# Kernel tuning notes

Hardware: AMD Instinct MI355X
Metric: run time of the kernel (lower is better)

Reference implementation:

```python
import jax, jax.numpy as jnp
import numpy as np

NF4_LUT = jnp.array([-1.0, -0.6961928009986877, -0.5250730514526367, -0.39491719007492065,
                     -0.28444138169288635, -0.18477343022823334, -0.08820830285549164, 0.0,
                     0.07107656449079514, 0.14263366162776947, 0.22430233657360077,
                     0.3203405737876892, 0.4407068192958832, 0.5905631184577942,
                     0.796090841293335, 1.0], dtype=jnp.float32)

BLOCK_SIZE = 64
OUT_FEATURES = 11008
IN_FEATURES = 4096


def dequantize_nf4(packed, absmax, out_shape):
    # packed: (O, I//2) int codes 0..255; absmax: (O, num_blocks)
    higher = packed // 16
    lower = packed % 16
    unpacked = jnp.stack([lower, higher], axis=-1).reshape(out_shape)  # (O, I)
    dequant = NF4_LUT[unpacked]  # LUT gather -> fp32 (O, I)
    O, I = out_shape
    # block-wise absmax scale
    dequant = (dequant.reshape(O, I // BLOCK_SIZE, BLOCK_SIZE) * absmax[:, :, None]).reshape(O, I)
    return dequant


def setup_inputs() -> dict:
    key = jax.random.key(0)
    k1, k2, k3, k4 = jax.random.split(key, 4)
    x = jax.random.normal(k1, (4, 2048, IN_FEATURES), dtype=jnp.float32)
    weight = jax.random.randint(k2, (OUT_FEATURES, IN_FEATURES // 2), 0, 256, dtype=jnp.int32)
    absmax = jax.random.uniform(k3, (OUT_FEATURES, IN_FEATURES // BLOCK_SIZE), dtype=jnp.float32)
    bias = jax.random.normal(k4, (OUT_FEATURES,), dtype=jnp.float32)
    return {"x": x, "weight": weight, "absmax": absmax, "bias": bias}


def reference(x, weight, absmax, bias):
    w = dequantize_nf4(weight, absmax, (OUT_FEATURES, IN_FEATURES))  # (O, I)
    # F.linear: y = x @ w.T + bias
    return jnp.einsum('bsi,oi->bso', x, w) + bias
```

## Files before the change

kernel.cpp:

```cpp
#include <hip/hip_runtime.h>

#define IN_F 4096
#define OUT_F 11008

typedef __attribute__((ext_vector_type(8))) short bf16x8;
typedef __attribute__((ext_vector_type(4))) float f32x4;
typedef __attribute__((ext_vector_type(4))) unsigned short us4;
typedef __attribute__((ext_vector_type(8))) unsigned short us8;

__device__ __forceinline__ unsigned short f2bf(float f) {
  unsigned int u = __float_as_uint(f);
  u += 0x7FFFu + ((u >> 16) & 1u);
  return (unsigned short)(u >> 16);
}

__global__ __launch_bounds__(256) void cvt_x(const float* __restrict__ X,
                                             unsigned short* __restrict__ Xb, int n8) {
  for (int i = blockIdx.x * blockDim.x + threadIdx.x; i < n8;
       i += gridDim.x * blockDim.x) {
    const float4 a = reinterpret_cast<const float4*>(X)[2 * i];
    const float4 b = reinterpret_cast<const float4*>(X)[2 * i + 1];
    us8 h;
    h[0] = f2bf(a.x); h[1] = f2bf(a.y); h[2] = f2bf(a.z); h[3] = f2bf(a.w);
    h[4] = f2bf(b.x); h[5] = f2bf(b.y); h[6] = f2bf(b.z); h[7] = f2bf(b.w);
    reinterpret_cast<us8*>(Xb)[i] = h;
  }
}

__global__ __launch_bounds__(256) void dequant_w(const int* __restrict__ Wp,
                                                 const float* __restrict__ Amax,
                                                 unsigned short* __restrict__ Wb, int n4) {
  __shared__ float lutS[16];
  if (threadIdx.x < 16) {
    const float lut[16] = {-1.0f, -0.6961928009986877f, -0.5250730514526367f,
        -0.39491719007492065f, -0.28444138169288635f, -0.18477343022823334f,
        -0.08820830285549164f, 0.0f, 0.07107656449079514f, 0.14263366162776947f,
        0.22430233657360077f, 0.3203405737876892f, 0.4407068192958832f,
        0.5905631184577942f, 0.796090841293335f, 1.0f};
    lutS[threadIdx.x] = lut[threadIdx.x];
  }
  __syncthreads();
  for (int i = blockIdx.x * blockDim.x + threadIdx.x; i < n4;
       i += gridDim.x * blockDim.x) {
    const int j = i * 4;
    const int row = j >> 11;
    const int coli = j & 2047;
    const float am = Amax[row * (IN_F / 64) + (coli >> 5)];
    const int4 pk = reinterpret_cast<const int4*>(Wp)[i];
    us8 h; int c;
    c = pk.x & 255; h[0] = f2bf(lutS[c & 15] * am); h[1] = f2bf(lutS[c >> 4] * am);
    c = pk.y & 255; h[2] = f2bf(lutS[c & 15] * am); h[3] = f2bf(lutS[c >> 4] * am);
    c = pk.z & 255; h[4] = f2bf(lutS[c & 15] * am); h[5] = f2bf(lutS[c >> 4] * am);
    c = pk.w & 255; h[6] = f2bf(lutS[c & 15] * am); h[7] = f2bf(lutS[c >> 4] * am);
    reinterpret_cast<us8*>(Wb)[i] = h;
  }
}

#define MF(a, b, c) __builtin_amdgcn_mfma_f32_16x16x32_bf16(a, b, c, 0, 0, 0)
#define GLDS(src, dst) __builtin_amdgcn_global_load_lds( \
    (const __attribute__((address_space(1))) void*)(src), \
    (__attribute__((address_space(3))) void*)(dst), 16, 0, 0)
#define FENCE asm volatile("" ::: "memory")
#define BAR do { FENCE; __builtin_amdgcn_s_barrier(); FENCE; } while (0)
#define VM8 asm volatile("s_waitcnt vmcnt(8)" ::: "memory")
#define VM4 asm volatile("s_waitcnt vmcnt(4)" ::: "memory")
#define VM0 asm volatile("s_waitcnt vmcnt(0)" ::: "memory")

__global__ __launch_bounds__(512, 2) void gemm256(
    const unsigned short* __restrict__ A,
    const unsigned short* __restrict__ B,
    const float* __restrict__ Bias, float* __restrict__ Out, int M) {
  extern __shared__ unsigned short sm[];
  unsigned short* LA = sm;
  unsigned short* LB = sm + 32768;

  const int tid = threadIdx.x;
  const int l = tid & 63;
  const int wid = tid >> 6;

  const int Mb = M / 256;
  const int Nb = OUT_F / 256;
  const int cpx = (Mb * Nb) >> 3;
  const int bid = (blockIdx.x & 7) * cpx + (blockIdx.x >> 3);
  const int m0 = (bid % Mb) * 256;
  const int n0 = (bid / Mb) * 256;

  const int rh = (l & 15) >> 1;
  const int cph = (((l & 1) << 2) + (l >> 4)) ^ rh;
  const int aoff = (((wid >> 2) * 64) + rh) * 64 + cph * 8;
  const int boff = (((wid & 3) * 32) + rh) * 64 + cph * 8;

  const int cc = (l & 7) ^ (l >> 3);
  const int R0 = 2 * (wid * 16 + (l >> 3)) + (cc >> 2);
  const long chb = (long)(cc & 3) * 16;
  const char* pA0 = (const char*)A + ((size_t)(m0 + R0) * IN_F) * 2 + chb;
  const char* pA1 = (const char*)A + ((size_t)(m0 + R0 + 16) * IN_F) * 2 + chb;
  const char* pB0 = (const char*)B + ((size_t)(n0 + R0) * IN_F) * 2 + chb;
  const char* pB1 = (const char*)B + ((size_t)(n0 + R0 + 16) * IN_F) * 2 + chb;
  const int dq0 = wid * 1024;
  const int dq1 = wid * 1024 + 512;

#define STAGE_A(tt) do { const int s_ = ((tt) & 3) * 8192; const size_t ko_ = (size_t)(tt) * 64; \
    GLDS(pA0 + ko_, LA + s_ + dq0); GLDS(pA1 + ko_, LA + s_ + dq1); } while (0)
#define STAGE_B(tt) do { const int s_ = ((tt) & 3) * 8192; const size_t ko_ = (size_t)(tt) * 64; \
    GLDS(pB0 + ko_, LB + s_ + dq0); GLDS(pB1 + ko_, LB + s_ + dq1); } while (0)

  f32x4 acc[8][4];
#pragma unroll
  for (int i = 0; i < 8; ++i)
#pragma unroll
    for (int j = 0; j < 4; ++j) acc[i][j] = {0.f, 0.f, 0.f, 0.f};

  STAGE_A(0); STAGE_B(0); STAGE_A(1); STAGE_B(1); STAGE_A(2); STAGE_B(2);

#define TILE(t, STG, VMW) do { \
  VMW; \
  BAR; \
  const int sb = ((t) & 3) * 8192; \
  bf16x8 a0, a1, a2, a3, a4, a5, a6, a7, b0, b1, b2, b3; \
  a0 = *(const bf16x8*)(LA + sb + aoff); \
  a1 = *(const bf16x8*)(LA + sb + aoff + 512); \
  a2 = *(const bf16x8*)(LA + sb + aoff + 1024); \
  a3 = *(const bf16x8*)(LA + sb + aoff + 1536); \
  b0 = *(const bf16x8*)(LB + sb + boff); \
  b1 = *(const bf16x8*)(LB + sb + boff + 512); \
  b2 = *(const bf16x8*)(LB + sb + boff + 1024); \
  b3 = *(const bf16x8*)(LB + sb + boff + 1536); \
  a4 = *(const bf16x8*)(LA + sb + aoff + 2048); \
  a5 = *(const bf16x8*)(LA + sb + aoff + 2560); \
  a6 = *(const bf16x8*)(LA + sb + aoff + 3072); \
  a7 = *(const bf16x8*)(LA + sb + aoff + 3584); \
  __builtin_amdgcn_s_setprio(1); \
  acc[0][0] = MF(a0, b0, acc[0][0]); acc[0][1] = MF(a0, b1, acc[0][1]); \
  acc[0][2] = MF(a0, b2, acc[0][2]); acc[0][3] = MF(a0, b3, acc[0][3]); \
  acc[1][0] = MF(a1, b0, acc[1][0]); acc[1][1] = MF(a1, b1, acc[1][1]); \
  acc[1][2] = MF(a1, b2, acc[1][2]); acc[1][3] = MF(a1, b3, acc[1][3]); \
  acc[2][0] = MF(a2, b0, acc[2][0]); acc[2][1] = MF(a2, b1, acc[2][1]); \
  acc[2][2] = MF(a2, b2, acc[2][2]); acc[2][3] = MF(a2, b3, acc[2][3]); \
  acc[3][0] = MF(a3, b0, acc[3][0]); acc[3][1] = MF(a3, b1, acc[3][1]); \
  acc[3][2] = MF(a3, b2, acc[3][2]); acc[3][3] = MF(a3, b3, acc[3][3]); \
  __builtin_amdgcn_s_setprio(0); \
  if (STG) { STAGE_A((t) + 3); STAGE_B((t) + 3); } \
  __builtin_amdgcn_s_setprio(1); \
  acc[4][0] = MF(a4, b0, acc[4][0]); acc[4][1] = MF(a4, b1, acc[4][1]); \
  acc[4][2] = MF(a4, b2, acc[4][2]); acc[4][3] = MF(a4, b3, acc[4][3]); \
  acc[5][0] = MF(a5, b0, acc[5][0]); acc[5][1] = MF(a5, b1, acc[5][1]); \
  acc[5][2] = MF(a5, b2, acc[5][2]); acc[5][3] = MF(a5, b3, acc[5][3]); \
  acc[6][0] = MF(a6, b0, acc[6][0]); acc[6][1] = MF(a6, b1, acc[6][1]); \
  acc[6][2] = MF(a6, b2, acc[6][2]); acc[6][3] = MF(a6, b3, acc[6][3]); \
  acc[7][0] = MF(a7, b0, acc[7][0]); acc[7][1] = MF(a7, b1, acc[7][1]); \
  acc[7][2] = MF(a7, b2, acc[7][2]); acc[7][3] = MF(a7, b3, acc[7][3]); \
  __builtin_amdgcn_s_setprio(0); \
} while (0)

  for (int t = 0; t < 125; ++t) { TILE(t, 1, VM8); }
  TILE(125, 0, VM8);
  TILE(126, 0, VM4);
  TILE(127, 0, VM0);

  const int crow = m0 + (wid >> 2) * 128 + ((l >> 4) << 2);
  const int ccol = n0 + (wid & 3) * 64 + (l & 15);
#pragma unroll
  for (int nf = 0; nf < 4; ++nf) {
    const float bv = Bias[ccol + nf * 16];
#pragma unroll
    for (int f = 0; f < 8; ++f)
#pragma unroll
      for (int rg = 0; rg < 4; ++rg)
        Out[(size_t)(crow + f * 16 + rg) * OUT_F + ccol + nf * 16] = acc[f][nf][rg] + bv;
  }
}

__global__ __launch_bounds__(256, 2) void nf4_gemm_fused(
    const float* __restrict__ X, const int* __restrict__ Wp,
    const float* __restrict__ Amax, const float* __restrict__ Bias,
    float* __restrict__ Out, int M) {
  __shared__ unsigned short As[128 * 64];
  __shared__ unsigned short Bs[128 * 64];
  __shared__ float lutS[16];

  const int t = threadIdx.x;
  const int l = t & 63;
  const int wid = t >> 6;

  if (t < 16) {
    const float lut[16] = {-1.0f, -0.6961928009986877f, -0.5250730514526367f,
        -0.39491719007492065f, -0.28444138169288635f, -0.18477343022823334f,
        -0.08820830285549164f, 0.0f, 0.07107656449079514f, 0.14263366162776947f,
        0.22430233657360077f, 0.3203405737876892f, 0.4407068192958832f,
        0.5905631184577942f, 0.796090841293335f, 1.0f};
    lutS[t] = lut[t];
  }

  const int ntile = OUT_F / 128;
  const int m0 = (blockIdx.x / ntile) * 128;
  const int n0 = (blockIdx.x % ntile) * 128;

  const int ar = t >> 4;
  const int ac4 = t & 15;
  const int br = t >> 3;
  const int bg = t & 7;
  const int wm = (wid >> 1) * 64;
  const int wn = (wid & 1) * 64;

  f32x4 acc[4][4];
#pragma unroll
  for (int i = 0; i < 4; ++i)
#pragma unroll
    for (int j = 0; j < 4; ++j) acc[i][j] = {0.f, 0.f, 0.f, 0.f};

  __syncthreads();

  for (int k0 = 0; k0 < IN_F; k0 += 64) {
#pragma unroll
    for (int p = 0; p < 8; ++p) {
      const int r = p * 16 + ar;
      const float4 v = *reinterpret_cast<const float4*>(
          X + (size_t)(m0 + r) * IN_F + k0 + ac4 * 4);
      us4 h;
      h[0] = f2bf(v.x); h[1] = f2bf(v.y); h[2] = f2bf(v.z); h[3] = f2bf(v.w);
      const int byte = r * 128 + ((ac4 * 8) ^ ((r & 7) << 4));
      *reinterpret_cast<us4*>(reinterpret_cast<char*>(As) + byte) = h;
    }
#pragma unroll
    for (int p = 0; p < 4; ++p) {
      const int r = p * 32 + br;
      const float amv = Amax[(size_t)(n0 + r) * (IN_F / 64) + (k0 >> 6)];
      const int4 pk = *reinterpret_cast<const int4*>(
          Wp + (size_t)(n0 + r) * (IN_F / 2) + (k0 >> 1) + bg * 4);
      us8 h;
      {
        int c;
        c = pk.x & 255; h[0] = f2bf(lutS[c & 15] * amv); h[1] = f2bf(lutS[c >> 4] * amv);
        c = pk.y & 255; h[2] = f2bf(lutS[c & 15] * amv); h[3] = f2bf(lutS[c >> 4] * amv);
        c = pk.z & 255; h[4] = f2bf(lutS[c & 15] * amv); h[5] = f2bf(lutS[c >> 4] * amv);
        c = pk.w & 255; h[6] = f2bf(lutS[c & 15] * amv); h[7] = f2bf(lutS[c >> 4] * amv);
      }
      const int byte = r * 128 + ((bg * 16) ^ ((r & 7) << 4));
      *reinterpret_cast<us8*>(reinterpret_cast<char*>(Bs) + byte) = h;
    }
    __syncthreads();

#pragma unroll
    for (int kk = 0; kk < 64; kk += 32) {
      bf16x8 af[4], bfv[4];
      const int kb = (kk + ((l >> 4) << 3)) * 2;
#pragma unroll
      for (int i = 0; i < 4; ++i) {
        const int row = wm + i * 16 + (l & 15);
        af[i] = *reinterpret_cast<const bf16x8*>(
            reinterpret_cast<const char*>(As) + row * 128 + (kb ^ ((row & 7) << 4)));
      }
#pragma unroll
      for (int j = 0; j < 4; ++j) {
        const int row = wn + j * 16 + (l & 15);
        bfv[j] = *reinterpret_cast<const bf16x8*>(
            reinterpret_cast<const char*>(Bs) + row * 128 + (kb ^ ((row & 7) << 4)));
      }
#pragma unroll
      for (int i = 0; i < 4; ++i)
#pragma unroll
        for (int j = 0; j < 4; ++j)
          acc[i][j] = __builtin_amdgcn_mfma_f32_16x16x32_bf16(af[i], bfv[j], acc[i][j], 0, 0, 0);
    }
    __syncthreads();
  }

  const int crow0 = m0 + wm + ((l >> 4) << 2);
  const int ccol0 = n0 + wn + (l & 15);
#pragma unroll
  for (int j = 0; j < 4; ++j) {
    const float bv = Bias[ccol0 + j * 16];
#pragma unroll
    for (int i = 0; i < 4; ++i)
#pragma unroll
      for (int rg = 0; rg < 4; ++rg)
        Out[(size_t)(crow0 + i * 16 + rg) * OUT_F + ccol0 + j * 16] = acc[i][j][rg] + bv;
  }
}

extern "C" void kernel_launch(void* const* d_in, const int* in_sizes, int n_in,
                              void* d_out, int out_size, void* d_ws, size_t ws_size,
                              hipStream_t stream) {
  const float* X = (const float*)d_in[0];
  const int* Wp = (const int*)d_in[1];
  const float* Amax = (const float*)d_in[2];
  const float* Bias = (const float*)d_in[3];
  float* Out = (float*)d_out;

  const int M = in_sizes[0] / IN_F;
  const size_t needX = (size_t)M * IN_F * 2;
  const size_t needW = (size_t)OUT_F * IN_F * 2;
  const int grid256 = (M / 256) * (OUT_F / 256);

  if (ws_size >= needX + needW && (M % 256) == 0 && (grid256 & 7) == 0) {
    unsigned short* Xb = (unsigned short*)d_ws;
    unsigned short* Wb = Xb + (size_t)M * IN_F;
    (void)hipFuncSetAttribute(reinterpret_cast<const void*>(gemm256),
                              hipFuncAttributeMaxDynamicSharedMemorySize, 131072);
    cvt_x<<<2048, 256, 0, stream>>>(X, Xb, M * (IN_F / 8));
    dequant_w<<<2048, 256, 0, stream>>>(Wp, Amax, Wb, OUT_F * (IN_F / 8));
    gemm256<<<grid256, 512, 131072, stream>>>(Xb, Wb, Bias, Out, M);
  } else {
    const int grid = (M / 128) * (OUT_F / 128);
    nf4_gemm_fused<<<grid, 256, 0, stream>>>(X, Wp, Amax, Bias, Out, M);
  }
}
```

Measured before the change: 850.4 us.

## Restructure bf16 GEMM main loop into 128-wide K tiles with interleaved staging

```diff
diff --git a/kernel.cpp b/kernel.cpp
--- a/kernel.cpp
+++ b/kernel.cpp
@@ -62,17 +62,18 @@
     (__attribute__((address_space(3))) void*)(dst), 16, 0, 0)
 #define FENCE asm volatile("" ::: "memory")
 #define BAR do { FENCE; __builtin_amdgcn_s_barrier(); FENCE; } while (0)
-#define VM8 asm volatile("s_waitcnt vmcnt(8)" ::: "memory")
-#define VM4 asm volatile("s_waitcnt vmcnt(4)" ::: "memory")
+#define VM6 asm volatile("s_waitcnt vmcnt(6)" ::: "memory")
 #define VM0 asm volatile("s_waitcnt vmcnt(0)" ::: "memory")
+#define VMNOP do {} while (0)
+#define P1 __builtin_amdgcn_s_setprio(1)
+#define P0 __builtin_amdgcn_s_setprio(0)
 
 __global__ __launch_bounds__(512, 2) void gemm256(
     const unsigned short* __restrict__ A,
     const unsigned short* __restrict__ B,
     const float* __restrict__ Bias, float* __restrict__ Out, int M) {
   extern __shared__ unsigned short sm[];
-  unsigned short* LA = sm;
-  unsigned short* LB = sm + 32768;
+  char* const smc = (char*)sm;
 
   const int tid = threadIdx.x;
   const int l = tid & 63;
@@ -85,25 +86,71 @@
   const int m0 = (bid % Mb) * 256;
   const int n0 = (bid / Mb) * 256;
 
-  const int rh = (l & 15) >> 1;
-  const int cph = (((l & 1) << 2) + (l >> 4)) ^ rh;
-  const int aoff = (((wid >> 2) * 64) + rh) * 64 + cph * 8;
-  const int boff = (((wid & 3) * 32) + rh) * 64 + cph * 8;
-
-  const int cc = (l & 7) ^ (l >> 3);
-  const int R0 = 2 * (wid * 16 + (l >> 3)) + (cc >> 2);
-  const long chb = (long)(cc & 3) * 16;
-  const char* pA0 = (const char*)A + ((size_t)(m0 + R0) * IN_F) * 2 + chb;
-  const char* pA1 = (const char*)A + ((size_t)(m0 + R0 + 16) * IN_F) * 2 + chb;
-  const char* pB0 = (const char*)B + ((size_t)(n0 + R0) * IN_F) * 2 + chb;
-  const char* pB1 = (const char*)B + ((size_t)(n0 + R0 + 16) * IN_F) * 2 + chb;
-  const int dq0 = wid * 1024;
-  const int dq1 = wid * 1024 + 512;
-
-#define STAGE_A(tt) do { const int s_ = ((tt) & 3) * 8192; const size_t ko_ = (size_t)(tt) * 64; \
-    GLDS(pA0 + ko_, LA + s_ + dq0); GLDS(pA1 + ko_, LA + s_ + dq1); } while (0)
-#define STAGE_B(tt) do { const int s_ = ((tt) & 3) * 8192; const size_t ko_ = (size_t)(tt) * 64; \
-    GLDS(pB0 + ko_, LB + s_ + dq0); GLDS(pB1 + ko_, LB + s_ + dq1); } while (0)
+  const int lv = (l & 15) * 64 + (((l >> 4) ^ ((l >> 2) & 3)) * 16);
+  const int aLane = (wid >> 2) * 8192 + lv;
+  const int bLane = 32768 + (wid & 3) * 4096 + lv;
+
+  const int rq = tid >> 2;
+  const int cs = (tid & 3) ^ ((tid >> 4) & 3);
+  const unsigned short* gAs = A + (size_t)(m0 + rq) * IN_F + cs * 8;
+  const unsigned short* gBs = B + (size_t)(n0 + rq) * IN_F + cs * 8;
+
+#define SA(t, kh) do { \
+    unsigned short* d_ = sm + (size_t)((((t) & 1) * 4096) + (kh) * 1024 + wid * 64) * 8; \
+    const unsigned short* s_ = gAs + (size_t)(t) * 64 + (kh) * 32; \
+    GLDS(s_, d_); GLDS(s_ + 524288, d_ + 4096); } while (0)
+#define SB(t, kh) do { \
+    unsigned short* d_ = sm + (size_t)((((t) & 1) * 4096) + 2048 + (kh) * 1024 + wid * 64) * 8; \
+    const unsigned short* s_ = gBs + (size_t)(t) * 64 + (kh) * 32; \
+    GLDS(s_, d_); GLDS(s_ + 524288, d_ + 4096); } while (0)
+
+#define RD_A(kh) do { const char* p_ = LAb + (kh) * 16384; \
+    a0 = *(const bf16x8*)(p_);        a1 = *(const bf16x8*)(p_ + 1024); \
+    a2 = *(const bf16x8*)(p_ + 2048); a3 = *(const bf16x8*)(p_ + 3072); \
+    a4 = *(const bf16x8*)(p_ + 4096); a5 = *(const bf16x8*)(p_ + 5120); \
+    a6 = *(const bf16x8*)(p_ + 6144); a7 = *(const bf16x8*)(p_ + 7168); } while (0)
+#define RD_B01(kh) do { const char* p_ = LBb + (kh) * 16384; \
+    b0 = *(const bf16x8*)(p_); b1 = *(const bf16x8*)(p_ + 1024); } while (0)
+#define RD_B23(kh) do { const char* p_ = LBb + (kh) * 16384 + 2048; \
+    b2 = *(const bf16x8*)(p_); b3 = *(const bf16x8*)(p_ + 1024); } while (0)
+
+#define MM16_01(B0, B1) do { \
+    acc[0][0]=MF(a0,B0,acc[0][0]); acc[0][1]=MF(a0,B1,acc[0][1]); \
+    acc[1][0]=MF(a1,B0,acc[1][0]); acc[1][1]=MF(a1,B1,acc[1][1]); \
+    acc[2][0]=MF(a2,B0,acc[2][0]); acc[2][1]=MF(a2,B1,acc[2][1]); \
+    acc[3][0]=MF(a3,B0,acc[3][0]); acc[3][1]=MF(a3,B1,acc[3][1]); \
+    acc[4][0]=MF(a4,B0,acc[4][0]); acc[4][1]=MF(a4,B1,acc[4][1]); \
+    acc[5][0]=MF(a5,B0,acc[5][0]); acc[5][1]=MF(a5,B1,acc[5][1]); \
+    acc[6][0]=MF(a6,B0,acc[6][0]); acc[6][1]=MF(a6,B1,acc[6][1]); \
+    acc[7][0]=MF(a7,B0,acc[7][0]); acc[7][1]=MF(a7,B1,acc[7][1]); } while (0)
+#define MM16_23(B2, B3) do { \
+    acc[0][2]=MF(a0,B2,acc[0][2]); acc[0][3]=MF(a0,B3,acc[0][3]); \
+    acc[1][2]=MF(a1,B2,acc[1][2]); acc[1][3]=MF(a1,B3,acc[1][3]); \
+    acc[2][2]=MF(a2,B2,acc[2][2]); acc[2][3]=MF(a2,B3,acc[2][3]); \
+    acc[3][2]=MF(a3,B2,acc[3][2]); acc[3][3]=MF(a3,B3,acc[3][3]); \
+    acc[4][2]=MF(a4,B2,acc[4][2]); acc[4][3]=MF(a4,B3,acc[4][3]); \
+    acc[5][2]=MF(a5,B2,acc[5][2]); acc[5][3]=MF(a5,B3,acc[5][3]); \
+    acc[6][2]=MF(a6,B2,acc[6][2]); acc[6][3]=MF(a6,B3,acc[6][3]); \
+    acc[7][2]=MF(a7,B2,acc[7][2]); acc[7][3]=MF(a7,B3,acc[7][3]); } while (0)
+
+#define KTILE(T, S1, S2, VMW) do { \
+    const char* LAb = smc + (((T) & 1) << 16) + aLane; \
+    const char* LBb = smc + (((T) & 1) << 16) + bLane; \
+    bf16x8 a0, a1, a2, a3, a4, a5, a6, a7, b0, b1, b2, b3; \
+    RD_A(0); RD_B01(0); \
+    if (S1) SB((T) + 1, 1); \
+    BAR; P1; MM16_01(b0, b1); P0; BAR; \
+    RD_B23(0); \
+    if (S2) SA((T) + 2, 0); \
+    BAR; P1; MM16_23(b2, b3); P0; BAR; \
+    RD_A(1); RD_B01(1); \
+    if (S2) SB((T) + 2, 0); \
+    BAR; P1; MM16_01(b0, b1); P0; BAR; \
+    RD_B23(1); \
+    if (S2) SA((T) + 2, 1); \
+    VMW; \
+    BAR; P1; MM16_23(b2, b3); P0; BAR; \
+  } while (0)
 
   f32x4 acc[8][4];
 #pragma unroll
@@ -111,52 +158,13 @@
 #pragma unroll
     for (int j = 0; j < 4; ++j) acc[i][j] = {0.f, 0.f, 0.f, 0.f};
 
-  STAGE_A(0); STAGE_B(0); STAGE_A(1); STAGE_B(1); STAGE_A(2); STAGE_B(2);
-
-#define TILE(t, STG, VMW) do { \
-  VMW; \
-  BAR; \
-  const int sb = ((t) & 3) * 8192; \
-  bf16x8 a0, a1, a2, a3, a4, a5, a6, a7, b0, b1, b2, b3; \
-  a0 = *(const bf16x8*)(LA + sb + aoff); \
-  a1 = *(const bf16x8*)(LA + sb + aoff + 512); \
-  a2 = *(const bf16x8*)(LA + sb + aoff + 1024); \
-  a3 = *(const bf16x8*)(LA + sb + aoff + 1536); \
-  b0 = *(const bf16x8*)(LB + sb + boff); \
-  b1 = *(const bf16x8*)(LB + sb + boff + 512); \
-  b2 = *(const bf16x8*)(LB + sb + boff + 1024); \
-  b3 = *(const bf16x8*)(LB + sb + boff + 1536); \
-  a4 = *(const bf16x8*)(LA + sb + aoff + 2048); \
-  a5 = *(const bf16x8*)(LA + sb + aoff + 2560); \
-  a6 = *(const bf16x8*)(LA + sb + aoff + 3072); \
-  a7 = *(const bf16x8*)(LA + sb + aoff + 3584); \
-  __builtin_amdgcn_s_setprio(1); \
-  acc[0][0] = MF(a0, b0, acc[0][0]); acc[0][1] = MF(a0, b1, acc[0][1]); \
-  acc[0][2] = MF(a0, b2, acc[0][2]); acc[0][3] = MF(a0, b3, acc[0][3]); \
-  acc[1][0] = MF(a1, b0, acc[1][0]); acc[1][1] = MF(a1, b1, acc[1][1]); \
-  acc[1][2] = MF(a1, b2, acc[1][2]); acc[1][3] = MF(a1, b3, acc[1][3]); \
-  acc[2][0] = MF(a2, b0, acc[2][0]); acc[2][1] = MF(a2, b1, acc[2][1]); \
-  acc[2][2] = MF(a2, b2, acc[2][2]); acc[2][3] = MF(a2, b3, acc[2][3]); \
-  acc[3][0] = MF(a3, b0, acc[3][0]); acc[3][1] = MF(a3, b1, acc[3][1]); \
-  acc[3][2] = MF(a3, b2, acc[3][2]); acc[3][3] = MF(a3, b3, acc[3][3]); \
-  __builtin_amdgcn_s_setprio(0); \
-  if (STG) { STAGE_A((t) + 3); STAGE_B((t) + 3); } \
-  __builtin_amdgcn_s_setprio(1); \
-  acc[4][0] = MF(a4, b0, acc[4][0]); acc[4][1] = MF(a4, b1, acc[4][1]); \
-  acc[4][2] = MF(a4, b2, acc[4][2]); acc[4][3] = MF(a4, b3, acc[4][3]); \
-  acc[5][0] = MF(a5, b0, acc[5][0]); acc[5][1] = MF(a5, b1, acc[5][1]); \
-  acc[5][2] = MF(a5, b2, acc[5][2]); acc[5][3] = MF(a5, b3, acc[5][3]); \
-  acc[6][0] = MF(a6, b0, acc[6][0]); acc[6][1] = MF(a6, b1, acc[6][1]); \
-  acc[6][2] = MF(a6, b2, acc[6][2]); acc[6][3] = MF(a6, b3, acc[6][3]); \
-  acc[7][0] = MF(a7, b0, acc[7][0]); acc[7][1] = MF(a7, b1, acc[7][1]); \
-  acc[7][2] = MF(a7, b2, acc[7][2]); acc[7][3] = MF(a7, b3, acc[7][3]); \
-  __builtin_amdgcn_s_setprio(0); \
-} while (0)
-
-  for (int t = 0; t < 125; ++t) { TILE(t, 1, VM8); }
-  TILE(125, 0, VM8);
-  TILE(126, 0, VM4);
-  TILE(127, 0, VM0);
+  SA(0, 0); SB(0, 0); SA(0, 1); SB(0, 1); SA(1, 0); SB(1, 0); SA(1, 1);
+  VM6;
+  BAR;
+
+  for (int T = 0; T < 62; ++T) { KTILE(T, 1, 1, VM6); }
+  KTILE(62, 1, 0, VM0);
+  KTILE(63, 0, 0, VMNOP);
 
   const int crow = m0 + (wid >> 2) * 128 + ((l >> 4) << 2);
   const int ccol = n0 + (wid & 3) * 64 + (l & 15);
```

Result: slower. 912.9 us (+7.3%).
